# Kernel tuning notes

Measured on AMD Instinct MI355X. Metric: run time of the kernel, lower is better.

The kernel has to match this reference:

```python
import jax, jax.numpy as jnp
import numpy as np

EPS = 1e-5
HID = 32
FUSED = 33 * 33 * 33  # 35937


def _subnet(x, gamma, beta, W1, b1, W2, b2, W3, b3):
    # BatchNorm1d in training mode: batch mean / biased variance
    mu = jnp.mean(x, axis=0)
    var = jnp.mean((x - mu) ** 2, axis=0)
    xn = (x - mu) / jnp.sqrt(var + EPS) * gamma + beta
    h = jax.nn.relu(xn @ W1 + b1)
    h = jax.nn.relu(h @ W2 + b2)
    return jax.nn.relu(h @ W3 + b3)


def _subnet_params(key, in_dim):
    ks = jax.random.split(key, 6)
    s_in = 1.0 / np.sqrt(in_dim)
    s_h = 1.0 / np.sqrt(HID)
    return dict(
        gamma=jnp.ones((in_dim,), jnp.float32),
        beta=jnp.zeros((in_dim,), jnp.float32),
        W1=jax.random.uniform(ks[0], (in_dim, HID), jnp.float32, -s_in, s_in),
        b1=jax.random.uniform(ks[1], (HID,), jnp.float32, -s_in, s_in),
        W2=jax.random.uniform(ks[2], (HID, HID), jnp.float32, -s_h, s_h),
        b2=jax.random.uniform(ks[3], (HID,), jnp.float32, -s_h, s_h),
        W3=jax.random.uniform(ks[4], (HID, HID), jnp.float32, -s_h, s_h),
        b3=jax.random.uniform(ks[5], (HID,), jnp.float32, -s_h, s_h),
    )


def setup_inputs() -> dict:
    key = jax.random.key(0)
    ks = jax.random.split(key, 10)
    B = 8192
    inp = {
        'US_x': jax.random.normal(ks[0], (B, 1024), jnp.float32),
        'CDFI_x': jax.random.normal(ks[1], (B, 1024), jnp.float32),
        'marker_x': jax.random.normal(ks[2], (B, 10), jnp.float32),
    }
    for pref, k, d in (('us', ks[3], 1024), ('cd', ks[4], 1024), ('mk', ks[5], 10)):
        for n, v in _subnet_params(k, d).items():
            inp[f'{pref}_{n}'] = v
    s1 = 1.0 / np.sqrt(FUSED)
    s2 = 1.0 / np.sqrt(33)
    inp['Wf1'] = jax.random.uniform(ks[6], (FUSED, 33), jnp.float32, -s1, s1)
    inp['bf1'] = jax.random.uniform(ks[7], (33,), jnp.float32, -s1, s1)
    inp['Wf2'] = jax.random.uniform(ks[8], (33, 5), jnp.float32, -s2, s2)
    inp['bf2'] = jax.random.uniform(ks[9], (5,), jnp.float32, -s2, s2)
    return inp


def reference(US_x, CDFI_x, marker_x,
              us_gamma, us_beta, us_W1, us_b1, us_W2, us_b2, us_W3, us_b3,
              cd_gamma, cd_beta, cd_W1, cd_b1, cd_W2, cd_b2, cd_W3, cd_b3,
              mk_gamma, mk_beta, mk_W1, mk_b1, mk_W2, mk_b2, mk_W3, mk_b3,
              Wf1, bf1, Wf2, bf2):
    B = US_x.shape[0]
    us_h = _subnet(US_x, us_gamma, us_beta, us_W1, us_b1, us_W2, us_b2, us_W3, us_b3)
    cd_h = _subnet(CDFI_x, cd_gamma, cd_beta, cd_W1, cd_b1, cd_W2, cd_b2, cd_W3, cd_b3)
    mk_h = _subnet(marker_x, mk_gamma, mk_beta, mk_W1, mk_b1, mk_W2, mk_b2, mk_W3, mk_b3)
    ones = jnp.ones((B, 1), jnp.float32)
    us1 = jnp.concatenate([ones, us_h], axis=1)   # [B,33]
    cd1 = jnp.concatenate([ones, cd_h], axis=1)   # [B,33]
    mk1 = jnp.concatenate([ones, mk_h], axis=1)   # [B,33]
    # fused[b,k,j,i] = mk1[b,k] * cd1[b,j] * us1[b,i]; flattened row-major
    fused = jnp.einsum('bk,bj,bi->bkji', mk1, cd1, us1).reshape(B, FUSED)
    h = jax.nn.relu(fused @ Wf1 + bf1)
    return jax.nn.sigmoid(h @ Wf2 + bf2)
```

## Files before the change

kernel.cpp:

```cpp
#include <hip/hip_runtime.h>
#include <hip/hip_bf16.h>
#include <math.h>

typedef __hip_bfloat16 bf16;
typedef __attribute__((ext_vector_type(4))) float f32x4;
typedef __attribute__((ext_vector_type(8))) short s16x8;

#define NB 8192
#define KP 1120
#define NP 1152

struct SubP {
    const float* x; const float* gamma; const float* beta;
    const float* W1; const float* b1; const float* W2; const float* b2;
    const float* W3; const float* b3;
    float* sum; float* sumsq; float* a; float* b1p; float* hout;
    int F;
};
struct SubP3 { SubP s[3]; };

__global__ void __launch_bounds__(256) stats3_kernel(SubP3 P) {
    const SubP p = P.s[blockIdx.z];
    int t = threadIdx.x;
    int row0 = blockIdx.x * 64;
    if (p.F == 1024) {
        f32x4 s = {0.f, 0.f, 0.f, 0.f}, s2 = {0.f, 0.f, 0.f, 0.f};
        const float* xp = p.x + (size_t)row0 * 1024 + t * 4;
        #pragma unroll 8
        for (int r = 0; r < 64; r++) {
            f32x4 v = *(const f32x4*)(xp + (size_t)r * 1024);
            s += v; s2 += v * v;
        }
        int f = t * 4;
        #pragma unroll
        for (int e = 0; e < 4; e++) {
            atomicAdd(&p.sum[f + e], s[e]);
            atomicAdd(&p.sumsq[f + e], s2[e]);
        }
    } else {
        __shared__ float ls[16], ls2[16];
        if (t < 16) { ls[t] = 0.f; ls2[t] = 0.f; }
        __syncthreads();
        int F = p.F;
        for (int idx = t; idx < 64 * F; idx += 256) {
            float v = p.x[(size_t)row0 * F + idx];
            int f = idx % 10;
            atomicAdd(&ls[f], v);
            atomicAdd(&ls2[f], v * v);
        }
        __syncthreads();
        if (t < F) { atomicAdd(&p.sum[t], ls[t]); atomicAdd(&p.sumsq[t], ls2[t]); }
    }
}

__global__ void prep3_kernel(SubP3 P) {
    const SubP p = P.s[blockIdx.y];
    int f0 = blockIdx.x * 32;
    if (f0 >= p.F) return;
    int t = threadIdx.x;
    __shared__ float c_sh[32];
    __shared__ float red[8][33];
    int fc = p.F - f0; if (fc > 32) fc = 32;
    if (t < 32) {
        float c = 0.f;
        if (t < fc) {
            int f = f0 + t;
            float mu  = p.sum[f]   * (1.f / 8192.f);
            float var = p.sumsq[f] * (1.f / 8192.f) - mu * mu;
            float a = p.gamma[f] * rsqrtf(var + 1e-5f);
            p.a[f] = a;
            c = p.beta[f] - mu * a;
        }
        c_sh[t] = c;
    }
    __syncthreads();
    int h = t & 31, g = t >> 5;
    float s = 0.f;
    for (int fi = g; fi < fc; fi += 8)
        s += c_sh[fi] * p.W1[(size_t)(f0 + fi) * 32 + h];
    red[g][h] = s;
    __syncthreads();
    if (t < 32) {
        float tot = 0.f;
        #pragma unroll
        for (int gg = 0; gg < 8; gg++) tot += red[gg][t];
        atomicAdd(&p.b1p[t], tot);
    }
}

__global__ void __launch_bounds__(256) subnet3_kernel(SubP3 P) {
    const SubP p = P.s[blockIdx.y];
    const int F = p.F;
    __shared__ float smem[8832];
    float* Red = smem;
    float* H1  = smem + 3456;
    float* W23 = smem + 4608;
    float* H2  = smem;

    int t = threadIdx.x;
    int row0 = blockIdx.x * 32;
    int kg = t >> 6;
    int lane = t & 63;
    int hg = lane & 7, h0 = hg * 4;
    int rg = (lane >> 3) & 3;
    int ks = lane >> 5;

    float acc[4][8] = {};

    if (F == 1024) {
        float* Xt = smem;
        float* Wt = smem + 4224;
        int xr = t >> 3, xc = (t & 7) * 16;
        int wk = t >> 1, wh = (t & 1) * 16;
        const float* xbase = p.x + (size_t)row0 * 1024;
        f32x4 xp[4], wp[4]; float av;
        #pragma unroll
        for (int i = 0; i < 4; i++) xp[i] = *(const f32x4*)&xbase[(size_t)xr * 1024 + xc + i * 4];
        #pragma unroll
        for (int i = 0; i < 4; i++) wp[i] = *(const f32x4*)&p.W1[(size_t)wk * 32 + wh + i * 4];
        av = p.a[wk];
        int kb = (kg * 2 + ks) * 16;
        for (int c = 0; c < 8; c++) {
            __syncthreads();
            #pragma unroll
            for (int i = 0; i < 4; i++) *(f32x4*)&Xt[xr * 132 + xc + i * 4] = xp[i];
            #pragma unroll
            for (int i = 0; i < 4; i++) *(f32x4*)&Wt[wk * 36 + wh + i * 4] = wp[i] * av;
            if (c < 7) {
                int k0 = (c + 1) * 128;
                #pragma unroll
                for (int i = 0; i < 4; i++) xp[i] = *(const f32x4*)&xbase[(size_t)xr * 1024 + k0 + xc + i * 4];
                #pragma unroll
                for (int i = 0; i < 4; i++) wp[i] = *(const f32x4*)&p.W1[(size_t)(k0 + wk) * 32 + wh + i * 4];
                av = p.a[k0 + wk];
            }
            __syncthreads();
            #pragma unroll
            for (int s = 0; s < 4; s++) {
                int kk = kb + s * 4;
                f32x4 wv[4], xv[8];
                #pragma unroll
                for (int j = 0; j < 4; j++)  wv[j]  = *(const f32x4*)&Wt[(kk + j) * 36 + h0];
                #pragma unroll
                for (int ri = 0; ri < 8; ri++) xv[ri] = *(const f32x4*)&Xt[(rg + 4 * ri) * 132 + kk];
                #pragma unroll
                for (int j = 0; j < 4; j++)
                    #pragma unroll
                    for (int hi = 0; hi < 4; hi++) {
                        float w = wv[j][hi];
                        #pragma unroll
                        for (int ri = 0; ri < 8; ri++)
                            acc[hi][ri] = fmaf(w, xv[ri][j], acc[hi][ri]);
                    }
            }
        }
    } else {
        float* Xt = smem;
        float* Wt = smem + 2176;
        int kbase = (kg * 2 + ks) * 8;
        for (int k0 = 0; k0 < F; k0 += 64) {
            int kc = F - k0; if (kc > 64) kc = 64;
            int kcp = (kc + 3) & ~3;
            __syncthreads();
            for (int idx = t; idx < 32 * kcp; idx += 256) {
                int r = idx / kcp, kk = idx - r * kcp;
                Xt[r * 68 + kk] = (kk < kc) ? p.x[(size_t)(row0 + r) * F + k0 + kk] : 0.f;
            }
            for (int idx = t; idx < kcp * 32; idx += 256) {
                int kk = idx >> 5, hh = idx & 31;
                Wt[kk * 36 + hh] = (kk < kc) ? p.a[k0 + kk] * p.W1[(size_t)(k0 + kk) * 32 + hh] : 0.f;
            }
            __syncthreads();
            #pragma unroll
            for (int s = 0; s < 2; s++) {
                int kk = kbase + s * 4;
                if (kk < kcp) {
                    f32x4 wv[4], xv[8];
                    #pragma unroll
                    for (int j = 0; j < 4; j++)  wv[j]  = *(const f32x4*)&Wt[(kk + j) * 36 + h0];
                    #pragma unroll
                    for (int ri = 0; ri < 8; ri++) xv[ri] = *(const f32x4*)&Xt[(rg + 4 * ri) * 68 + kk];
                    #pragma unroll
                    for (int j = 0; j < 4; j++)
                        #pragma unroll
                        for (int hi = 0; hi < 4; hi++) {
                            float w = wv[j][hi];
                            #pragma unroll
                            for (int ri = 0; ri < 8; ri++)
                                acc[hi][ri] = fmaf(w, xv[ri][j], acc[hi][ri]);
                        }
                }
            }
        }
    }
    #pragma unroll
    for (int hi = 0; hi < 4; hi++)
        #pragma unroll
        for (int ri = 0; ri < 8; ri++)
            acc[hi][ri] += __shfl_xor(acc[hi][ri], 32);
    __syncthreads();
    if (kg > 0 && ks == 0) {
        #pragma unroll
        for (int ri = 0; ri < 8; ri++) {
            int r = rg + 4 * ri;
            f32x4 v = {acc[0][ri], acc[1][ri], acc[2][ri], acc[3][ri]};
            *(f32x4*)&Red[(kg - 1) * 1152 + r * 36 + h0] = v;
        }
    }
    for (int idx = t; idx < 1024; idx += 256) W23[(idx >> 5) * 33 + (idx & 31)] = p.W2[idx];
    __syncthreads();
    if (kg == 0 && ks == 0) {
        f32x4 b;
        #pragma unroll
        for (int hi = 0; hi < 4; hi++) b[hi] = p.b1[h0 + hi] + p.b1p[h0 + hi];
        #pragma unroll
        for (int ri = 0; ri < 8; ri++) {
            int r = rg + 4 * ri;
            f32x4 v = {acc[0][ri], acc[1][ri], acc[2][ri], acc[3][ri]};
            #pragma unroll
            for (int pp = 0; pp < 3; pp++)
                v += *(const f32x4*)&Red[pp * 1152 + r * 36 + h0];
            v += b;
            #pragma unroll
            for (int hi = 0; hi < 4; hi++)
                H1[r * 36 + h0 + hi] = fmaxf(v[hi], 0.f);
        }
    }
    __syncthreads();
    int h = t & 31, rq = t >> 5;
    {
        float a2[4] = {};
        for (int q = 0; q < 32; q++) {
            float w = W23[q * 33 + h];
            #pragma unroll
            for (int i = 0; i < 4; i++) a2[i] += H1[(rq * 4 + i) * 36 + q] * w;
        }
        float bv = p.b2[h];
        #pragma unroll
        for (int i = 0; i < 4; i++) H2[(rq * 4 + i) * 36 + h] = fmaxf(a2[i] + bv, 0.f);
    }
    __syncthreads();
    for (int idx = t; idx < 1024; idx += 256) W23[(idx >> 5) * 33 + (idx & 31)] = p.W3[idx];
    __syncthreads();
    {
        float a3[4] = {};
        for (int q = 0; q < 32; q++) {
            float w = W23[q * 33 + h];
            #pragma unroll
            for (int i = 0; i < 4; i++) a3[i] += H2[(rq * 4 + i) * 36 + q] * w;
        }
        float bv = p.b3[h];
        #pragma unroll
        for (int i = 0; i < 4; i++)
            p.hout[(size_t)(row0 + rq * 4 + i) * 32 + h] = fmaxf(a3[i] + bv, 0.f);
    }
}

__global__ void build_both(const float* __restrict__ mk_h, const float* __restrict__ us_h,
                           bf16* __restrict__ p1,
                           const float* __restrict__ Wf1, bf16* __restrict__ W2t) {
    int blk = blockIdx.x;
    int t = threadIdx.x;
    if (blk < NB) {
        int b = blk;
        __shared__ float mk1[33], us1[33];
        if (t == 0) { mk1[0] = 1.f; us1[0] = 1.f; }
        if (t < 32) mk1[t + 1] = mk_h[(size_t)b * 32 + t];
        else if (t < 64) us1[t - 31] = us_h[(size_t)b * 32 + (t - 32)];
        __syncthreads();
        if (t < 140) {
            int base = t * 8;
            s16x8 v;
            #pragma unroll
            for (int e = 0; e < 8; e++) {
                int idx = base + e;
                float val = 0.f;
                if (idx < 1089) {
                    int k = idx / 33, i = idx - k * 33;
                    val = mk1[k] * us1[i];
                }
                __hip_bfloat16 hb = __float2bfloat16(val);
                v[e] = *(short*)&hb;
            }
            *(s16x8*)(p1 + (size_t)b * KP + base) = v;
        }
    } else {
        int kj = blk - NB;
        int k = kj / 33, j = kj - k * 33;
        __shared__ float tile[1089];
        const float* src = Wf1 + (size_t)k * 35937 + (size_t)j * 1089;
        for (int idx = t; idx < 1089; idx += 192) tile[idx] = src[idx];
        __syncthreads();
        for (int idx = t; idx < 1089; idx += 192) {
            int o = idx / 33, i = idx - o * 33;
            W2t[(size_t)(j * 33 + o) * KP + k * 33 + i] = __float2bfloat16(tile[i * 33 + o]);
        }
        if (k == 0) {
            bf16 z = __float2bfloat16(0.f);
            for (int idx = t; idx < 33 * 31; idx += 192) {
                int o = idx / 31, kkp = 1089 + idx - o * 31;
                W2t[(size_t)(j * 33 + o) * KP + kkp] = z;
            }
        }
    }
}

__global__ void __launch_bounds__(256) gemm_kernel(const bf16* __restrict__ A,
                                                   const bf16* __restrict__ Bt,
                                                   bf16* __restrict__ S) {
    __shared__ __align__(16) bf16 As[128 * 32];
    __shared__ __align__(16) bf16 Bs[128 * 32];
    int t = threadIdx.x;
    int m0 = blockIdx.x * 128;
    int n0 = blockIdx.y * 128;
    int wave = t >> 6, lane = t & 63;
    int wm = (wave & 1) * 64, wn = (wave >> 1) * 64;
    int fr = lane & 15;
    int kg = (lane >> 4) * 8;

    int lr = lane >> 2;
    int lk = (lane & 3) * 8;
    const bf16* Ag = A  + (size_t)(m0 + wave * 32 + lr) * KP + lk;
    const bf16* Bg = Bt + (size_t)(n0 + wave * 32 + lr) * KP + lk;
    bf16* AsW = As + wave * 32 * 32;
    bf16* BsW = Bs + wave * 32 * 32;

    f32x4 acc[4][4] = {};

    for (int k0 = 0; k0 < KP; k0 += 32) {
        __syncthreads();
        __builtin_amdgcn_global_load_lds(
            (const __attribute__((address_space(1))) void*)(Ag + k0),
            (__attribute__((address_space(3))) void*)(AsW), 16, 0, 0);
        __builtin_amdgcn_global_load_lds(
            (const __attribute__((address_space(1))) void*)(Ag + k0 + 16 * KP),
            (__attribute__((address_space(3))) void*)(AsW + 16 * 32), 16, 0, 0);
        __builtin_amdgcn_global_load_lds(
            (const __attribute__((address_space(1))) void*)(Bg + k0),
            (__attribute__((address_space(3))) void*)(BsW), 16, 0, 0);
        __builtin_amdgcn_global_load_lds(
            (const __attribute__((address_space(1))) void*)(Bg + k0 + 16 * KP),
            (__attribute__((address_space(3))) void*)(BsW + 16 * 32), 16, 0, 0);
        __syncthreads();
        s16x8 bfr[4];
        #pragma unroll
        for (int nt = 0; nt < 4; nt++)
            bfr[nt] = *(const s16x8*)(Bs + (wn + nt * 16 + fr) * 32 + kg);
        #pragma unroll
        for (int mt = 0; mt < 4; mt++) {
            s16x8 af = *(const s16x8*)(As + (wm + mt * 16 + fr) * 32 + kg);
            #pragma unroll
            for (int nt = 0; nt < 4; nt++)
                acc[mt][nt] = __builtin_amdgcn_mfma_f32_16x16x32_bf16(af, bfr[nt], acc[mt][nt], 0, 0, 0);
        }
    }
    int col = lane & 15, rowg = (lane >> 4) * 4;
    #pragma unroll
    for (int mt = 0; mt < 4; mt++)
        #pragma unroll
        for (int nt = 0; nt < 4; nt++)
            #pragma unroll
            for (int r = 0; r < 4; r++) {
                int gr = m0 + wm + mt * 16 + rowg + r;
                int gc = n0 + wn + nt * 16 + col;
                S[(size_t)gr * NP + gc] = __float2bfloat16(acc[mt][nt][r]);
            }
}

__global__ void __launch_bounds__(256) epilogue_kernel(const bf16* __restrict__ S,
                                const float* __restrict__ cd_h,
                                const float* __restrict__ bf1, const float* __restrict__ Wf2,
                                const float* __restrict__ bf2, float* __restrict__ out) {
    int w = threadIdx.x >> 6;
    int lane = threadIdx.x & 63;
    int b = blockIdx.x * 4 + w;
    __shared__ __align__(16) unsigned short Sl[4][1152];
    __shared__ float cdsh[4][33];
    __shared__ float hsh[4][40];
    const bf16* Srow = S + (size_t)b * NP;
    #pragma unroll
    for (int pass = 0; pass < 3; pass++) {
        int idx = lane + pass * 64;
        if (idx < 144)
            *(s16x8*)&Sl[w][idx * 8] = *(const s16x8*)(Srow + idx * 8);
    }
    if (lane == 0) cdsh[w][0] = 1.f;
    if (lane < 32) cdsh[w][lane + 1] = cd_h[(size_t)b * 32 + lane];
    __syncthreads();
    if (lane < 33) {
        float acc = bf1[lane];
        #pragma unroll 3
        for (int j = 0; j < 33; j++) {
            unsigned short sv = Sl[w][j * 33 + lane];
            acc += cdsh[w][j] * __bfloat162float(*(bf16*)&sv);
        }
        hsh[w][lane] = fmaxf(acc, 0.f);
    }
    __syncthreads();
    if (lane < 5) {
        float o = bf2[lane];
        for (int q = 0; q < 33; q++) o += hsh[w][q] * Wf2[q * 5 + lane];
        out[(size_t)b * 5 + lane] = 1.f / (1.f + expf(-o));
    }
}

extern "C" void kernel_launch(void* const* d_in, const int* in_sizes, int n_in,
                              void* d_out, int out_size, void* d_ws, size_t ws_size,
                              hipStream_t stream) {
    const float* US_x     = (const float*)d_in[0];
    const float* CDFI_x   = (const float*)d_in[1];
    const float* marker_x = (const float*)d_in[2];
    const float* Wf1      = (const float*)d_in[27];
    const float* bf1      = (const float*)d_in[28];
    const float* Wf2      = (const float*)d_in[29];
    const float* bf2      = (const float*)d_in[30];
    float* out = (float*)d_out;

    char* ws = (char*)d_ws;
    size_t off = 0;
    auto alloc = [&](size_t bytes) -> void* {
        void* p = ws + off;
        off = (off + bytes + 255) & ~(size_t)255;
        return p;
    };

    float* stat_big = (float*)alloc(3 * 2176 * sizeof(float));
    float* a_buf[3], *h_buf[3];
    for (int i = 0; i < 3; i++) {
        a_buf[i] = (float*)alloc(1024 * 4);
        h_buf[i] = (float*)alloc((size_t)NB * 32 * 4);
    }
    bf16*  p1   = (bf16*)alloc((size_t)NB * KP * 2);
    bf16*  W2t  = (bf16*)alloc((size_t)NP * KP * 2);
    bf16*  S    = (bf16*)alloc((size_t)NB * NP * 2);

    SubP3 P;
    const float* xs[3] = {US_x, CDFI_x, marker_x};
    int Fs[3] = {1024, 1024, 10};
    for (int i = 0; i < 3; i++) {
        int base = 3 + i * 8;
        P.s[i].x     = xs[i];
        P.s[i].gamma = (const float*)d_in[base + 0];
        P.s[i].beta  = (const float*)d_in[base + 1];
        P.s[i].W1    = (const float*)d_in[base + 2];
        P.s[i].b1    = (const float*)d_in[base + 3];
        P.s[i].W2    = (const float*)d_in[base + 4];
        P.s[i].b2    = (const float*)d_in[base + 5];
        P.s[i].W3    = (const float*)d_in[base + 6];
        P.s[i].b3    = (const float*)d_in[base + 7];
        P.s[i].sum   = stat_big + i * 2176;
        P.s[i].sumsq = stat_big + i * 2176 + 1024;
        P.s[i].b1p   = stat_big + i * 2176 + 2048;
        P.s[i].a     = a_buf[i];
        P.s[i].hout  = h_buf[i];
        P.s[i].F     = Fs[i];
    }

    float* us_h = h_buf[0];
    float* cd_h = h_buf[1];
    float* mk_h = h_buf[2];

    hipMemsetAsync(stat_big, 0, 3 * 2176 * sizeof(float), stream);

    stats3_kernel<<<dim3(128, 1, 3), 256, 0, stream>>>(P);
    prep3_kernel<<<dim3(32, 3), 256, 0, stream>>>(P);
    subnet3_kernel<<<dim3(256, 3), 256, 0, stream>>>(P);

    build_both<<<NB + 1089, 192, 0, stream>>>(mk_h, us_h, p1, Wf1, W2t);

    gemm_kernel<<<dim3(NB / 128, NP / 128), 256, 0, stream>>>(p1, W2t, S);

    epilogue_kernel<<<NB / 4, 256, 0, stream>>>(S, cd_h, bf1, Wf2, bf2, out);
}
```

Measured before the change: 261.8 us.

## Double GEMM K-tile to 64 with XOR-swizzled LDS layout

Result: no change. 264.1 us (+0.9%).

```diff
diff --git a/kernel.cpp b/kernel.cpp
--- a/kernel.cpp
+++ b/kernel.cpp
@@ -7,7 +7,7 @@
 typedef __attribute__((ext_vector_type(8))) short s16x8;
 
 #define NB 8192
-#define KP 1120
+#define KP 1152
 #define NP 1152
 
 struct SubP {
@@ -268,7 +268,7 @@
         if (t < 32) mk1[t + 1] = mk_h[(size_t)b * 32 + t];
         else if (t < 64) us1[t - 31] = us_h[(size_t)b * 32 + (t - 32)];
         __syncthreads();
-        if (t < 140) {
+        if (t < 144) {
             int base = t * 8;
             s16x8 v;
             #pragma unroll
@@ -297,8 +297,8 @@
         }
         if (k == 0) {
             bf16 z = __float2bfloat16(0.f);
-            for (int idx = t; idx < 33 * 31; idx += 192) {
-                int o = idx / 31, kkp = 1089 + idx - o * 31;
+            for (int idx = t; idx < 33 * 63; idx += 192) {
+                int o = idx / 63, kkp = 1089 + idx - o * 63;
                 W2t[(size_t)(j * 33 + o) * KP + kkp] = z;
             }
         }
@@ -308,50 +308,55 @@
 __global__ void __launch_bounds__(256) gemm_kernel(const bf16* __restrict__ A,
                                                    const bf16* __restrict__ Bt,
                                                    bf16* __restrict__ S) {
-    __shared__ __align__(16) bf16 As[128 * 32];
-    __shared__ __align__(16) bf16 Bs[128 * 32];
+    __shared__ __align__(16) bf16 As[128 * 64];
+    __shared__ __align__(16) bf16 Bs[128 * 64];
     int t = threadIdx.x;
     int m0 = blockIdx.x * 128;
     int n0 = blockIdx.y * 128;
     int wave = t >> 6, lane = t & 63;
     int wm = (wave & 1) * 64, wn = (wave >> 1) * 64;
     int fr = lane & 15;
-    int kg = (lane >> 4) * 8;
-
-    int lr = lane >> 2;
-    int lk = (lane & 3) * 8;
-    const bf16* Ag = A  + (size_t)(m0 + wave * 32 + lr) * KP + lk;
-    const bf16* Bg = Bt + (size_t)(n0 + wave * 32 + lr) * KP + lk;
-    bf16* AsW = As + wave * 32 * 32;
-    bf16* BsW = Bs + wave * 32 * 32;
+    int kgi = lane >> 4;
+
+    int srow = lane >> 3;
+    int sc = (lane & 7) ^ srow;
+    const bf16* Ag = A  + (size_t)(m0 + srow) * KP + sc * 8;
+    const bf16* Bg = Bt + (size_t)(n0 + srow) * KP + sc * 8;
 
     f32x4 acc[4][4] = {};
 
-    for (int k0 = 0; k0 < KP; k0 += 32) {
-        __syncthreads();
-        __builtin_amdgcn_global_load_lds(
-            (const __attribute__((address_space(1))) void*)(Ag + k0),
-            (__attribute__((address_space(3))) void*)(AsW), 16, 0, 0);
-        __builtin_amdgcn_global_load_lds(
-            (const __attribute__((address_space(1))) void*)(Ag + k0 + 16 * KP),
-            (__attribute__((address_space(3))) void*)(AsW + 16 * 32), 16, 0, 0);
-        __builtin_amdgcn_global_load_lds(
-            (const __attribute__((address_space(1))) void*)(Bg + k0),
-            (__attribute__((address_space(3))) void*)(BsW), 16, 0, 0);
-        __builtin_amdgcn_global_load_lds(
-            (const __attribute__((address_space(1))) void*)(Bg + k0 + 16 * KP),
-            (__attribute__((address_space(3))) void*)(BsW + 16 * 32), 16, 0, 0);
-        __syncthreads();
-        s16x8 bfr[4];
-        #pragma unroll
-        for (int nt = 0; nt < 4; nt++)
-            bfr[nt] = *(const s16x8*)(Bs + (wn + nt * 16 + fr) * 32 + kg);
-        #pragma unroll
-        for (int mt = 0; mt < 4; mt++) {
-            s16x8 af = *(const s16x8*)(As + (wm + mt * 16 + fr) * 32 + kg);
+    for (int k0 = 0; k0 < KP; k0 += 64) {
+        __syncthreads();
+        #pragma unroll
+        for (int i = 0; i < 4; i++) {
+            int base = wave * 32 + i * 8;
+            __builtin_amdgcn_global_load_lds(
+                (const __attribute__((address_space(1))) void*)(Ag + (size_t)base * KP + k0),
+                (__attribute__((address_space(3))) void*)(As + base * 64), 16, 0, 0);
+        }
+        #pragma unroll
+        for (int i = 0; i < 4; i++) {
+            int base = wave * 32 + i * 8;
+            __builtin_amdgcn_global_load_lds(
+                (const __attribute__((address_space(1))) void*)(Bg + (size_t)base * KP + k0),
+                (__attribute__((address_space(3))) void*)(Bs + base * 64), 16, 0, 0);
+        }
+        __syncthreads();
+        #pragma unroll
+        for (int h = 0; h < 2; h++) {
+            int c = h * 4 + kgi;
+            int pofs = (c ^ (fr & 7)) * 8;
+            s16x8 bfr[4];
             #pragma unroll
             for (int nt = 0; nt < 4; nt++)
-                acc[mt][nt] = __builtin_amdgcn_mfma_f32_16x16x32_bf16(af, bfr[nt], acc[mt][nt], 0, 0, 0);
+                bfr[nt] = *(const s16x8*)(Bs + (wn + nt * 16 + fr) * 64 + pofs);
+            #pragma unroll
+            for (int mt = 0; mt < 4; mt++) {
+                s16x8 af = *(const s16x8*)(As + (wm + mt * 16 + fr) * 64 + pofs);
+                #pragma unroll
+                for (int nt = 0; nt < 4; nt++)
+                    acc[mt][nt] = __builtin_amdgcn_mfma_f32_16x16x32_bf16(af, bfr[nt], acc[mt][nt], 0, 0, 0);
+            }
         }
     }
     int col = lane & 15, rowg = (lane >> 4) * 4;
```

## Shrink GEMM M-tile to 64, swizzle LDS layout, pad K to 1152

Applied to the files above, without the earlier changes.

Measured after the change: 261.9 us. No clear change (+0.0%).

```diff
diff --git a/kernel.cpp b/kernel.cpp
--- a/kernel.cpp
+++ b/kernel.cpp
@@ -7,7 +7,7 @@
 typedef __attribute__((ext_vector_type(8))) short s16x8;
 
 #define NB 8192
-#define KP 1120
+#define KP 1152
 #define NP 1152
 
 struct SubP {
@@ -268,7 +268,7 @@
         if (t < 32) mk1[t + 1] = mk_h[(size_t)b * 32 + t];
         else if (t < 64) us1[t - 31] = us_h[(size_t)b * 32 + (t - 32)];
         __syncthreads();
-        if (t < 140) {
+        if (t < 144) {
             int base = t * 8;
             s16x8 v;
             #pragma unroll
@@ -297,8 +297,8 @@
         }
         if (k == 0) {
             bf16 z = __float2bfloat16(0.f);
-            for (int idx = t; idx < 33 * 31; idx += 192) {
-                int o = idx / 31, kkp = 1089 + idx - o * 31;
+            for (int idx = t; idx < 33 * 63; idx += 192) {
+                int o = idx / 63, kkp = 1089 + idx - o * 63;
                 W2t[(size_t)(j * 33 + o) * KP + kkp] = z;
             }
         }
@@ -308,55 +308,54 @@
 __global__ void __launch_bounds__(256) gemm_kernel(const bf16* __restrict__ A,
                                                    const bf16* __restrict__ Bt,
                                                    bf16* __restrict__ S) {
-    __shared__ __align__(16) bf16 As[128 * 32];
+    __shared__ __align__(16) bf16 As[64 * 32];
     __shared__ __align__(16) bf16 Bs[128 * 32];
     int t = threadIdx.x;
-    int m0 = blockIdx.x * 128;
+    int m0 = blockIdx.x * 64;
     int n0 = blockIdx.y * 128;
     int wave = t >> 6, lane = t & 63;
-    int wm = (wave & 1) * 64, wn = (wave >> 1) * 64;
+    int wm = (wave & 1) * 32, wn = (wave >> 1) * 64;
     int fr = lane & 15;
-    int kg = (lane >> 4) * 8;
-
-    int lr = lane >> 2;
-    int lk = (lane & 3) * 8;
-    const bf16* Ag = A  + (size_t)(m0 + wave * 32 + lr) * KP + lk;
-    const bf16* Bg = Bt + (size_t)(n0 + wave * 32 + lr) * KP + lk;
-    bf16* AsW = As + wave * 32 * 32;
+    int kgi = lane >> 4;
+
+    int sr = lane >> 2, sp = lane & 3;
+    int sc = sp ^ (sr & 3);
+    const bf16* AgW = A  + (size_t)(m0 + wave * 16 + sr) * KP + sc * 8;
+    const bf16* BgW = Bt + (size_t)(n0 + wave * 32 + sr) * KP + sc * 8;
+    bf16* AsW = As + wave * 16 * 32;
     bf16* BsW = Bs + wave * 32 * 32;
 
-    f32x4 acc[4][4] = {};
+    f32x4 acc[2][4] = {};
 
     for (int k0 = 0; k0 < KP; k0 += 32) {
         __syncthreads();
         __builtin_amdgcn_global_load_lds(
-            (const __attribute__((address_space(1))) void*)(Ag + k0),
+            (const __attribute__((address_space(1))) void*)(AgW + k0),
             (__attribute__((address_space(3))) void*)(AsW), 16, 0, 0);
         __builtin_amdgcn_global_load_lds(
-            (const __attribute__((address_space(1))) void*)(Ag + k0 + 16 * KP),
-            (__attribute__((address_space(3))) void*)(AsW + 16 * 32), 16, 0, 0);
-        __builtin_amdgcn_global_load_lds(
-            (const __attribute__((address_space(1))) void*)(Bg + k0),
+            (const __attribute__((address_space(1))) void*)(BgW + k0),
             (__attribute__((address_space(3))) void*)(BsW), 16, 0, 0);
         __builtin_amdgcn_global_load_lds(
-            (const __attribute__((address_space(1))) void*)(Bg + k0 + 16 * KP),
+            (const __attribute__((address_space(1))) void*)(BgW + k0 + (size_t)16 * KP),
             (__attribute__((address_space(3))) void*)(BsW + 16 * 32), 16, 0, 0);
         __syncthreads();
-        s16x8 bfr[4];
+        int pofs = (kgi ^ (fr & 3)) * 8;
+        s16x8 af[2], bq[4];
+        #pragma unroll
+        for (int mt = 0; mt < 2; mt++)
+            af[mt] = *(const s16x8*)(As + (wm + mt * 16 + fr) * 32 + pofs);
         #pragma unroll
         for (int nt = 0; nt < 4; nt++)
-            bfr[nt] = *(const s16x8*)(Bs + (wn + nt * 16 + fr) * 32 + kg);
-        #pragma unroll
-        for (int mt = 0; mt < 4; mt++) {
-            s16x8 af = *(const s16x8*)(As + (wm + mt * 16 + fr) * 32 + kg);
+            bq[nt] = *(const s16x8*)(Bs + (wn + nt * 16 + fr) * 32 + pofs);
+        #pragma unroll
+        for (int mt = 0; mt < 2; mt++)
             #pragma unroll
             for (int nt = 0; nt < 4; nt++)
-                acc[mt][nt] = __builtin_amdgcn_mfma_f32_16x16x32_bf16(af, bfr[nt], acc[mt][nt], 0, 0, 0);
-        }
+                acc[mt][nt] = __builtin_amdgcn_mfma_f32_16x16x32_bf16(af[mt], bq[nt], acc[mt][nt], 0, 0, 0);
     }
     int col = lane & 15, rowg = (lane >> 4) * 4;
     #pragma unroll
-    for (int mt = 0; mt < 4; mt++)
+    for (int mt = 0; mt < 2; mt++)
         #pragma unroll
         for (int nt = 0; nt < 4; nt++)
             #pragma unroll
@@ -468,7 +467,7 @@
 
     build_both<<<NB + 1089, 192, 0, stream>>>(mk_h, us_h, p1, Wf1, W2t);
 
-    gemm_kernel<<<dim3(NB / 128, NP / 128), 256, 0, stream>>>(p1, W2t, S);
+    gemm_kernel<<<dim3(128, 9), 256, 0, stream>>>(p1, W2t, S);
 
     epilogue_kernel<<<NB / 4, 256, 0, stream>>>(S, cd_h, bf1, Wf2, bf2, out);
 }
```
